# Kernel optimization log

Hardware: AMD Instinct MI355X
Metric: run time of the kernel (lower is better)

Reference implementation:

```python
import jax, jax.numpy as jnp
import numpy as np

THRESH = 8000.0  # saturating partial-sum accumulator threshold (thresh=8000 in source)
GROUP = 128      # channel chunk size used by split_tensor_* helpers
EPS = 1e-5

def binarize(x):
    # sign() forward with straight-through estimator (standard BinarizeConv2d behavior)
    return x + jax.lax.stop_gradient(jnp.sign(x) - x)

def psum_conv3x3(x, w):
    """3x3 'same' conv computed as 9 shifted-window partial sums per 128-channel
    group, with the running accumulator saturated to [-THRESH, THRESH] after each
    partial sum (emulating a low-bit hardware accumulator).
    x: [B, C, H, W]; w: [O, C, 3, 3] -> out [B, O, H, W]."""
    B, C, H, W = x.shape
    O = w.shape[0]
    xp = jnp.pad(x, ((0, 0), (0, 0), (1, 1), (1, 1)))
    acc = jnp.zeros((B, O, H, W), dtype=x.dtype)
    n_groups = C // GROUP
    for g in range(n_groups):
        xg = xp[:, g * GROUP:(g + 1) * GROUP]
        wg = w[:, g * GROUP:(g + 1) * GROUP]
        # split_tensor ordering: x1..x9 vary row (dim2) fastest, then col (dim3)
        for col in range(3):
            for row in range(3):
                part = jnp.einsum('bchw,oc->bohw',
                                  xg[:, :, row:row + H, col:col + W],
                                  wg[:, :, row, col])
                acc = jnp.clip(acc + part, -THRESH, THRESH)
    return acc

def batchnorm(x, gamma, beta, mean, var):
    inv = gamma / jnp.sqrt(var + EPS)
    return x * inv[None, :, None, None] + (beta - mean * inv)[None, :, None, None]

def setup_inputs() -> dict:
    key = jax.random.key(0)
    ks = jax.random.split(key, 12)
    B, C, H, W = 64, 128, 56, 56
    return {
        'x': jax.random.normal(ks[0], (B, C, H, W), jnp.float32),
        'w1': jax.random.normal(ks[1], (C, C, 3, 3), jnp.float32),
        'w2': jax.random.normal(ks[2], (C, C, 3, 3), jnp.float32),
        'gamma1': jax.random.uniform(ks[3], (C,), jnp.float32, 0.5, 1.5),
        'beta1': jax.random.normal(ks[4], (C,), jnp.float32) * 0.1,
        'mean1': jax.random.normal(ks[5], (C,), jnp.float32),
        'var1': jax.random.uniform(ks[6], (C,), jnp.float32, 0.5, 1.5),
        'gamma2': jax.random.uniform(ks[7], (C,), jnp.float32, 0.5, 1.5),
        'beta2': jax.random.normal(ks[8], (C,), jnp.float32) * 0.1,
        'mean2': jax.random.normal(ks[9], (C,), jnp.float32),
        'var2': jax.random.uniform(ks[10], (C,), jnp.float32, 0.5, 1.5),
    }

def reference(x, w1, w2, gamma1, beta1, mean1, var1, gamma2, beta2, mean2, var2):
    residual = x
    out = psum_conv3x3(binarize(x), binarize(w1))
    out = batchnorm(out, gamma1, beta1, mean1, var1)
    out = jnp.clip(out, -1.0, 1.0)  # hardtanh
    out = psum_conv3x3(binarize(out), binarize(w2))
    out = batchnorm(out, gamma2, beta2, mean2, var2)
    out = out + residual
    out = jnp.clip(out, -1.0, 1.0)
    return out
```

## Files before the change

kernel.cpp:

```cpp
#include <hip/hip_runtime.h>
#include <cstdint>
#include <cstddef>


typedef int      v4i __attribute__((ext_vector_type(4)));
typedef float    v4f __attribute__((ext_vector_type(4)));
typedef unsigned int v2u __attribute__((ext_vector_type(2)));

constexpr int B = 64, C = 128, H = 56, W = 56;
constexpr int HP = H + 2, WP = W + 2;
constexpr int PIX = H * W;
constexpr int M = B * H * W;
constexpr int NTILES = M / 256;
constexpr int TPX = NTILES / 8;

constexpr size_t XS_BYTES = (size_t)B * HP * WP * C;
constexpr size_t XS1_OFF = 0;
constexpr size_t XS2_OFF = XS_BYTES;
constexpr size_t WF_BYTES = 18 * 8192;
constexpr size_t WF1_OFF = 2 * XS_BYTES;
constexpr size_t WF2_OFF = WF1_OFF + WF_BYTES;
constexpr size_t BNP_OFF = WF2_OFF + WF_BYTES;

__global__ __launch_bounds__(256) void zero_halo(int8_t* __restrict__ xs1,
                                                 int8_t* __restrict__ xs2) {
    int b = blockIdx.x;
    int t = threadIdx.x;
    size_t ib = (size_t)b * HP * WP * C;
#pragma unroll
    for (int a = 0; a < 2; ++a) {
        uint32_t* p = (uint32_t*)((a ? xs2 : xs1) + ib);
        const int ROWD = WP * C / 4;
        for (int i = t; i < ROWD; i += 256) {
            p[i] = 0;
            p[(HP - 1) * ROWD + i] = 0;
        }
        for (int i = t; i < 56 * 2 * 32; i += 256) {
            int r = i >> 6;
            int side = (i >> 5) & 1;
            int j = i & 31;
            p[((r + 1) * WP + side * (WP - 1)) * (C / 4) + j] = 0;
        }
    }
}

__global__ __launch_bounds__(256) void prep_x(const float* __restrict__ x,
                                              int8_t* __restrict__ xs) {
    __shared__ uint32_t tl[256 * 33];
    int t = threadIdx.x;
    int m = blockIdx.x * 256 + t;
    int b_ = m / PIX, hw = m % PIX;
    const float* xp = x + (size_t)b_ * C * PIX + hw;
#pragma unroll
    for (int c4 = 0; c4 < 32; ++c4) {
        uint32_t v = 0;
#pragma unroll
        for (int j = 0; j < 4; ++j) {
            float f = xp[(size_t)(c4 * 4 + j) * PIX];
            v |= ((uint32_t)(uint8_t)(int8_t)((f > 0.f) - (f < 0.f))) << (8 * j);
        }
        tl[t * 33 + c4] = v;
    }
    __syncthreads();
    int pl = t >> 3, co = t & 7;
#pragma unroll
    for (int pass = 0; pass < 8; ++pass) {
        int p = pass * 32 + pl;
        int mg = blockIdx.x * 256 + p;
        int b2 = mg / PIX, hw2 = mg % PIX, h2 = hw2 / W, w2 = hw2 % W;
        size_t ob = ((size_t)(b2 * HP + h2 + 1) * WP + (w2 + 1)) * C + co * 16;
        v4i val;
#pragma unroll
        for (int k = 0; k < 4; ++k) val[k] = (int)tl[p * 33 + co * 4 + k];
        *(v4i*)(xs + ob) = val;
    }
}

__global__ __launch_bounds__(256) void prep_w(
    const float* __restrict__ w1, const float* __restrict__ w2,
    const float* __restrict__ g1, const float* __restrict__ be1,
    const float* __restrict__ mu1, const float* __restrict__ va1,
    const float* __restrict__ g2, const float* __restrict__ be2,
    const float* __restrict__ mu2, const float* __restrict__ va2,
    int8_t* __restrict__ wf1, int8_t* __restrict__ wf2,
    float* __restrict__ bnp) {
    int t = blockIdx.x * 256 + threadIdx.x;
    if (t < 256) {
        int o = t & 127;
        if (t < 128) {
            float inv = g1[o] / sqrtf(va1[o] + 1e-5f);
            bnp[o]       = inv;
            bnp[128 + o] = __fsub_rn(be1[o], __fmul_rn(mu1[o], inv));
        } else {
            float inv = g2[o] / sqrtf(va2[o] + 1e-5f);
            bnp[256 + o] = inv;
            bnp[384 + o] = __fsub_rn(be2[o], __fmul_rn(mu2[o], inv));
        }
    }
    if (t >= 2 * 18 * 8 * 64) return;
    int lane = t & 63;
    int nsub = (t >> 6) & 7;
    int kh   = (t >> 9) & 1;
    int tap  = (t >> 10) % 9;
    int which = (t >> 10) / 9;
    const float* w = which ? w2 : w1;
    int8_t* wf = which ? wf2 : wf1;
    int o = (lane & 15) * 8 + nsub;
    int cbase = kh * 64 + (lane >> 4) * 16;
    int r = tap / 3, s = tap % 3;
    int8_t frag[16];
#pragma unroll
    for (int j = 0; j < 16; ++j) {
        float f = w[((size_t)(o * C + cbase + j) * 3 + r) * 3 + s];
        frag[j] = (int8_t)((f > 0.f) - (f < 0.f));
    }
    *(v4i*)(wf + (size_t)(((tap * 2 + kh) * 8 + nsub) * 64 + lane) * 16) =
        *(const v4i*)frag;
}

template <int PHASE>
__global__ __launch_bounds__(512, 1) void conv_bin(
    const int8_t* __restrict__ xs,
    const int8_t* __restrict__ wf,
    const float* __restrict__ bnp,
    const float* __restrict__ xres,
    int8_t* __restrict__ xs_next,
    float* __restrict__ out)
{
    __shared__ int8_t wlds[18 * 8192];
    int t = threadIdx.x, lane = t & 63, wv = t >> 6;
    int quad = lane >> 4, l15 = lane & 15;

    {
        const v4i* g = (const v4i*)wf;
        v4i* l = (v4i*)wlds;
        for (int i = t; i < 18 * 512; i += 512) l[i] = g[i];
    }
    float binv[8], btt[8];
    {
        int o0 = (PHASE == 1 ? 0 : 256) + l15 * 8;
        int o1 = (PHASE == 1 ? 128 : 384) + l15 * 8;
#pragma unroll
        for (int n = 0; n < 8; ++n) { binv[n] = bnp[o0 + n]; btt[n] = bnp[o1 + n]; }
    }
    __syncthreads();

    int xcd = blockIdx.x & 7, local = blockIdx.x >> 3;
    for (int tloc = local; tloc < TPX; tloc += 32) {
        int tile = xcd * TPX + tloc;
        int mwave = tile * 256 + wv * 32;
        int abase[2];
#pragma unroll
        for (int rg = 0; rg < 2; ++rg) {
            int ma = mwave + rg * 16 + l15;
            int wa = ma % W; int ta = ma / W; int ha = ta % H; int ba = ta / H;
            abase[rg] = ((ba * HP + ha) * WP + wa) * C + quad * 16;
        }

        v4i acc[2][8];
#pragma unroll
        for (int rg = 0; rg < 2; ++rg)
#pragma unroll
            for (int n = 0; n < 8; ++n) acc[rg][n] = (v4i)0;

        v4i a[2];
#pragma unroll
        for (int rg = 0; rg < 2; ++rg) a[rg] = *(const v4i*)(xs + abase[rg]);

#pragma unroll 1
        for (int step = 0; step < 18; ++step) {
            v4i an[2];
            if (step + 1 < 18) {
                int nt = (step + 1) >> 1, nk = (step + 1) & 1;
                int aoff = ((nt / 3) * WP + (nt % 3)) * C + nk * 64;
#pragma unroll
                for (int rg = 0; rg < 2; ++rg)
                    an[rg] = *(const v4i*)(xs + abase[rg] + aoff);
            }
            const int8_t* lb = wlds + step * 8192;
#pragma unroll
            for (int n = 0; n < 8; ++n) {
                v4i bf = *(const v4i*)(lb + ((n * 64 + lane) << 4));
#pragma unroll
                for (int rg = 0; rg < 2; ++rg)
                    acc[rg][n] = __builtin_amdgcn_mfma_i32_16x16x64_i8(
                        a[rg], bf, acc[rg][n], 0, 0, 0);
            }
#pragma unroll
            for (int rg = 0; rg < 2; ++rg) a[rg] = an[rg];
        }

#pragma unroll
        for (int rg = 0; rg < 2; ++rg) {
            int m0 = mwave + rg * 16 + quad * 4;
            int w0 = m0 % W; int t0 = m0 / W; int h0 = t0 % H; int b0 = t0 / H;
            if (PHASE == 1) {
                int base = ((b0 * HP + h0 + 1) * WP + (w0 + 1)) * C + l15 * 8;
#pragma unroll
                for (int i = 0; i < 4; ++i) {
                    uint32_t lo = 0, hi = 0;
#pragma unroll
                    for (int n = 0; n < 8; ++n) {
                        float y = __fadd_rn(__fmul_rn((float)acc[rg][n][i], binv[n]), btt[n]);
                        uint32_t sb = (uint8_t)(int8_t)((y > 0.f) - (y < 0.f));
                        if (n < 4) lo |= sb << (8 * n);
                        else       hi |= sb << (8 * (n - 4));
                    }
                    v2u pk; pk[0] = lo; pk[1] = hi;
                    *(v2u*)(xs_next + base + i * C) = pk;
                }
            } else {
                int pixb = b0 * C * PIX + h0 * W + w0;
#pragma unroll
                for (int n = 0; n < 8; ++n) {
                    int idx = pixb + (l15 * 8 + n) * PIX;
                    v4f r = *(const v4f*)(xres + idx);
                    v4f z;
#pragma unroll
                    for (int i = 0; i < 4; ++i) {
                        float y = __fadd_rn(__fmul_rn((float)acc[rg][n][i], binv[n]), btt[n]);
                        float v = __fadd_rn(y, r[i]);
                        z[i] = fminf(fmaxf(v, -1.f), 1.f);
                    }
                    *(v4f*)(out + idx) = z;
                }
            }
        }
    }
}

extern "C" void kernel_launch(void* const* d_in, const int* in_sizes, int n_in,
                              void* d_out, int out_size, void* d_ws, size_t ws_size,
                              hipStream_t stream) {
    const float* x   = (const float*)d_in[0];
    const float* w1  = (const float*)d_in[1];
    const float* w2  = (const float*)d_in[2];
    const float* g1  = (const float*)d_in[3];
    const float* be1 = (const float*)d_in[4];
    const float* mu1 = (const float*)d_in[5];
    const float* va1 = (const float*)d_in[6];
    const float* g2  = (const float*)d_in[7];
    const float* be2 = (const float*)d_in[8];
    const float* mu2 = (const float*)d_in[9];
    const float* va2 = (const float*)d_in[10];

    int8_t* ws  = (int8_t*)d_ws;
    int8_t* xs1 = ws + XS1_OFF;
    int8_t* xs2 = ws + XS2_OFF;
    int8_t* wf1 = ws + WF1_OFF;
    int8_t* wf2 = ws + WF2_OFF;
    float*  bnp = (float*)(ws + BNP_OFF);

    zero_halo<<<B, 256, 0, stream>>>(xs1, xs2);
    prep_x<<<M / 256, 256, 0, stream>>>(x, xs1);
    prep_w<<<(2 * 18 * 8 * 64 + 255) / 256, 256, 0, stream>>>(
        w1, w2, g1, be1, mu1, va1, g2, be2, mu2, va2, wf1, wf2, bnp);

    conv_bin<1><<<256, 512, 0, stream>>>(xs1, wf1, bnp, nullptr, xs2, nullptr);
    conv_bin<2><<<256, 512, 0, stream>>>(xs2, wf2, bnp, x, nullptr, (float*)d_out);
}
```

Measured before the change: 350.9 us.

## Double-buffer MFMA operands, reorder weight slots, balance tail tiles, use nontemporal IO

The conv loop now double-buffers both the activation fragments and the LDS weight fragments two steps at a time, so loads for the next step are in flight while MFMAs run. Weight slots are reordered so each row's taps are contiguous. The tail tiles (TPX=98 per XCD, not divisible by 32 blocks) are split into half-size wave chunks spread over more blocks to reduce load imbalance. Other changes: halo zeroing runs on more blocks, and the fp32 input, residual and output use nontemporal loads and stores. More operand registers are live at once, which raises register pressure.

Measured after the change: 327.0 us. 1.07x faster.

```diff
diff --git a/kernel.cpp b/kernel.cpp
--- a/kernel.cpp
+++ b/kernel.cpp
@@ -22,20 +22,26 @@
 constexpr size_t WF2_OFF = WF1_OFF + WF_BYTES;
 constexpr size_t BNP_OFF = WF2_OFF + WF_BYTES;
 
+__device__ __forceinline__ int step_aoff(int st) {
+    int r = st / 6, kh = (st / 3) & 1, s = st % 3;
+    return (r * WP + s) * C + kh * 64;
+}
+
 __global__ __launch_bounds__(256) void zero_halo(int8_t* __restrict__ xs1,
                                                  int8_t* __restrict__ xs2) {
-    int b = blockIdx.x;
-    int t = threadIdx.x;
+    int b = blockIdx.x >> 2;
+    int q = blockIdx.x & 3;
+    int t = q * 256 + threadIdx.x;
     size_t ib = (size_t)b * HP * WP * C;
 #pragma unroll
     for (int a = 0; a < 2; ++a) {
         uint32_t* p = (uint32_t*)((a ? xs2 : xs1) + ib);
         const int ROWD = WP * C / 4;
-        for (int i = t; i < ROWD; i += 256) {
+        for (int i = t; i < ROWD; i += 1024) {
             p[i] = 0;
             p[(HP - 1) * ROWD + i] = 0;
         }
-        for (int i = t; i < 56 * 2 * 32; i += 256) {
+        for (int i = t; i < 56 * 2 * 32; i += 1024) {
             int r = i >> 6;
             int side = (i >> 5) & 1;
             int j = i & 31;
@@ -56,7 +62,7 @@
         uint32_t v = 0;
 #pragma unroll
         for (int j = 0; j < 4; ++j) {
-            float f = xp[(size_t)(c4 * 4 + j) * PIX];
+            float f = __builtin_nontemporal_load(xp + (size_t)(c4 * 4 + j) * PIX);
             v |= ((uint32_t)(uint8_t)(int8_t)((f > 0.f) - (f < 0.f))) << (8 * j);
         }
         tl[t * 33 + c4] = v;
@@ -108,14 +114,117 @@
     int o = (lane & 15) * 8 + nsub;
     int cbase = kh * 64 + (lane >> 4) * 16;
     int r = tap / 3, s = tap % 3;
+    int slot = r * 6 + kh * 3 + s;
     int8_t frag[16];
 #pragma unroll
     for (int j = 0; j < 16; ++j) {
         float f = w[((size_t)(o * C + cbase + j) * 3 + r) * 3 + s];
         frag[j] = (int8_t)((f > 0.f) - (f < 0.f));
     }
-    *(v4i*)(wf + (size_t)(((tap * 2 + kh) * 8 + nsub) * 64 + lane) * 16) =
+    *(v4i*)(wf + (size_t)((slot * 8 + nsub) * 64 + lane) * 16) =
         *(const v4i*)frag;
+}
+
+template <int PHASE, int RG>
+__device__ __forceinline__ void do_tile(
+    int mwave, const int8_t* __restrict__ xs, const int8_t* wlds,
+    const float* binv, const float* btt, int lane, int quad, int l15,
+    const float* __restrict__ xres, int8_t* __restrict__ xs_next,
+    float* __restrict__ out)
+{
+    int abase[RG];
+#pragma unroll
+    for (int rg = 0; rg < RG; ++rg) {
+        int ma = mwave + rg * 16 + l15;
+        int wa = ma % W; int ta = ma / W; int ha = ta % H; int ba = ta / H;
+        abase[rg] = ((ba * HP + ha) * WP + wa) * C + quad * 16;
+    }
+
+    v4i acc[RG][8];
+#pragma unroll
+    for (int rg = 0; rg < RG; ++rg)
+#pragma unroll
+        for (int n = 0; n < 8; ++n) acc[rg][n] = (v4i)0;
+
+    v4i a0[RG], a1[RG], bf0[8], bf1[8];
+#pragma unroll
+    for (int rg = 0; rg < RG; ++rg) a0[rg] = *(const v4i*)(xs + abase[rg]);
+#pragma unroll
+    for (int n = 0; n < 8; ++n)
+        bf0[n] = *(const v4i*)(wlds + ((n * 64 + lane) << 4));
+
+#pragma unroll 1
+    for (int s2 = 0; s2 < 18; s2 += 2) {
+        {
+            int aoff = step_aoff(s2 + 1);
+            const int8_t* lb = wlds + (s2 + 1) * 8192;
+#pragma unroll
+            for (int rg = 0; rg < RG; ++rg)
+                a1[rg] = *(const v4i*)(xs + abase[rg] + aoff);
+#pragma unroll
+            for (int n = 0; n < 8; ++n)
+                bf1[n] = *(const v4i*)(lb + ((n * 64 + lane) << 4));
+        }
+#pragma unroll
+        for (int n = 0; n < 8; ++n)
+#pragma unroll
+            for (int rg = 0; rg < RG; ++rg)
+                acc[rg][n] = __builtin_amdgcn_mfma_i32_16x16x64_i8(
+                    a0[rg], bf0[n], acc[rg][n], 0, 0, 0);
+        if (s2 + 2 < 18) {
+            int aoff = step_aoff(s2 + 2);
+            const int8_t* lb = wlds + (s2 + 2) * 8192;
+#pragma unroll
+            for (int rg = 0; rg < RG; ++rg)
+                a0[rg] = *(const v4i*)(xs + abase[rg] + aoff);
+#pragma unroll
+            for (int n = 0; n < 8; ++n)
+                bf0[n] = *(const v4i*)(lb + ((n * 64 + lane) << 4));
+        }
+#pragma unroll
+        for (int n = 0; n < 8; ++n)
+#pragma unroll
+            for (int rg = 0; rg < RG; ++rg)
+                acc[rg][n] = __builtin_amdgcn_mfma_i32_16x16x64_i8(
+                    a1[rg], bf1[n], acc[rg][n], 0, 0, 0);
+    }
+
+#pragma unroll
+    for (int rg = 0; rg < RG; ++rg) {
+        int m0 = mwave + rg * 16 + quad * 4;
+        int w0 = m0 % W; int t0 = m0 / W; int h0 = t0 % H; int b0 = t0 / H;
+        if (PHASE == 1) {
+            int base = ((b0 * HP + h0 + 1) * WP + (w0 + 1)) * C + l15 * 8;
+#pragma unroll
+            for (int i = 0; i < 4; ++i) {
+                uint32_t lo = 0, hi = 0;
+#pragma unroll
+                for (int n = 0; n < 8; ++n) {
+                    float y = __fadd_rn(__fmul_rn((float)acc[rg][n][i], binv[n]), btt[n]);
+                    uint32_t sb = (uint8_t)(int8_t)((y > 0.f) - (y < 0.f));
+                    if (n < 4) lo |= sb << (8 * n);
+                    else       hi |= sb << (8 * (n - 4));
+                }
+                v2u pk; pk[0] = lo; pk[1] = hi;
+                *(v2u*)(xs_next + base + i * C) = pk;
+            }
+        } else {
+            int pixb = b0 * C * PIX + h0 * W + w0;
+#pragma unroll
+            for (int n = 0; n < 8; ++n) {
+                int idx = pixb + (l15 * 8 + n) * PIX;
+                v4f r = __builtin_nontemporal_load((const v4f*)(xres + idx));
+                v4f z;
+#pragma unroll
+                for (int i = 0; i < 4; ++i) {
+                    float y = __fadd_rn(__fmul_rn((float)acc[rg][n][i], binv[n]), btt[n]);
+                    float v = __fadd_rn(y, r[i]);
+                    z[i] = fminf(fmaxf(v, -1.f), 1.f);
+                }
+                __builtin_nontemporal_store(z, (v4f*)(out + idx));
+            }
+        }
+    }
 }
 
 template <int PHASE>
@@ -146,86 +255,17 @@
     __syncthreads();
 
     int xcd = blockIdx.x & 7, local = blockIdx.x >> 3;
-    for (int tloc = local; tloc < TPX; tloc += 32) {
+#pragma unroll 1
+    for (int tloc = local; tloc < 96; tloc += 32) {
         int tile = xcd * TPX + tloc;
-        int mwave = tile * 256 + wv * 32;
-        int abase[2];
-#pragma unroll
-        for (int rg = 0; rg < 2; ++rg) {
-            int ma = mwave + rg * 16 + l15;
-            int wa = ma % W; int ta = ma / W; int ha = ta % H; int ba = ta / H;
-            abase[rg] = ((ba * HP + ha) * WP + wa) * C + quad * 16;
-        }
-
-        v4i acc[2][8];
-#pragma unroll
-        for (int rg = 0; rg < 2; ++rg)
-#pragma unroll
-            for (int n = 0; n < 8; ++n) acc[rg][n] = (v4i)0;
-
-        v4i a[2];
-#pragma unroll
-        for (int rg = 0; rg < 2; ++rg) a[rg] = *(const v4i*)(xs + abase[rg]);
-
-#pragma unroll 1
-        for (int step = 0; step < 18; ++step) {
-            v4i an[2];
-            if (step + 1 < 18) {
-                int nt = (step + 1) >> 1, nk = (step + 1) & 1;
-                int aoff = ((nt / 3) * WP + (nt % 3)) * C + nk * 64;
-#pragma unroll
-                for (int rg = 0; rg < 2; ++rg)
-                    an[rg] = *(const v4i*)(xs + abase[rg] + aoff);
-            }
-            const int8_t* lb = wlds + step * 8192;
-#pragma unroll
-            for (int n = 0; n < 8; ++n) {
-                v4i bf = *(const v4i*)(lb + ((n * 64 + lane) << 4));
-#pragma unroll
-                for (int rg = 0; rg < 2; ++rg)
-                    acc[rg][n] = __builtin_amdgcn_mfma_i32_16x16x64_i8(
-                        a[rg], bf, acc[rg][n], 0, 0, 0);
-            }
-#pragma unroll
-            for (int rg = 0; rg < 2; ++rg) a[rg] = an[rg];
-        }
-
-#pragma unroll
-        for (int rg = 0; rg < 2; ++rg) {
-            int m0 = mwave + rg * 16 + quad * 4;
-            int w0 = m0 % W; int t0 = m0 / W; int h0 = t0 % H; int b0 = t0 / H;
-            if (PHASE == 1) {
-                int base = ((b0 * HP + h0 + 1) * WP + (w0 + 1)) * C + l15 * 8;
-#pragma unroll
-                for (int i = 0; i < 4; ++i) {
-                    uint32_t lo = 0, hi = 0;
-#pragma unroll
-                    for (int n = 0; n < 8; ++n) {
-                        float y = __fadd_rn(__fmul_rn((float)acc[rg][n][i], binv[n]), btt[n]);
-                        uint32_t sb = (uint8_t)(int8_t)((y > 0.f) - (y < 0.f));
-                        if (n < 4) lo |= sb << (8 * n);
-                        else       hi |= sb << (8 * (n - 4));
-                    }
-                    v2u pk; pk[0] = lo; pk[1] = hi;
-                    *(v2u*)(xs_next + base + i * C) = pk;
-                }
-            } else {
-                int pixb = b0 * C * PIX + h0 * W + w0;
-#pragma unroll
-                for (int n = 0; n < 8; ++n) {
-                    int idx = pixb + (l15 * 8 + n) * PIX;
-                    v4f r = *(const v4f*)(xres + idx);
-                    v4f z;
-#pragma unroll
-                    for (int i = 0; i < 4; ++i) {
-                        float y = __fadd_rn(__fmul_rn((float)acc[rg][n][i], binv[n]), btt[n]);
-                        float v = __fadd_rn(y, r[i]);
-                        z[i] = fminf(fmaxf(v, -1.f), 1.f);
-                    }
-                    *(v4f*)(out + idx) = z;
-                }
-            }
-        }
+        do_tile<PHASE, 2>(tile * 256 + wv * 32, xs, wlds, binv, btt,
+                          lane, quad, l15, xres, xs_next, out);
+    }
+    if (local < 4) {
+        int tile = xcd * TPX + 96 + (local >> 1);
+        int mw = tile * 256 + (local & 1) * 128 + wv * 16;
+        do_tile<PHASE, 1>(mw, xs, wlds, binv, btt,
+                          lane, quad, l15, xres, xs_next, out);
     }
 }
 
@@ -251,7 +291,7 @@
     int8_t* wf2 = ws + WF2_OFF;
     float*  bnp = (float*)(ws + BNP_OFF);
 
-    zero_halo<<<B, 256, 0, stream>>>(xs1, xs2);
+    zero_halo<<<256, 256, 0, stream>>>(xs1, xs2);
     prep_x<<<M / 256, 256, 0, stream>>>(x, xs1);
     prep_w<<<(2 * 18 * 8 * 64 + 255) / 256, 256, 0, stream>>>(
         w1, w2, g1, be1, mu1, va1, g2, be2, mu2, va2, wf1, wf2, bnp);
```
